# Optimization experiments

Measured on AMD Instinct MI355X. Metric: run time of the kernel, lower is better.

The kernel has to match this reference:

```python
import jax, jax.numpy as jnp
import numpy as np
from jax import lax

B, S, W = 64, 64, 12          # batch, sentences, words-per-sentence (max_seq)
V, SYM, HID = 32000, 128, 256  # vocab, symbol_size, hidden_size
E, R = 64, 32                  # entity_size, role_size
EPS = 1e-5


def _mlp(x, W1, b1, W2, b2):
    # equation 'b...e,er->b...r' is a matmul on the last axis; tanh hidden, linear out
    return jnp.tanh(x @ W1 + b1) @ W2 + b2


def _ln(x, g, b):
    mu = jnp.mean(x, axis=-1, keepdims=True)
    var = jnp.mean(jnp.square(x - mu), axis=-1, keepdims=True)
    return (x - mu) * lax.rsqrt(var + EPS) * g + b


def setup_inputs() -> dict:
    key = jax.random.key(0)
    ks = jax.random.split(key, 24)
    s_in = 1.0 / np.sqrt(SYM)
    s_h = 1.0 / np.sqrt(HID)
    inp = {
        "story": jax.random.randint(ks[0], (B, S, W), 0, V),
        "query": jax.random.randint(ks[1], (B, W), 0, V),
        "word_embed": jax.random.uniform(ks[2], (V, SYM), jnp.float32, -0.1, 0.1),
        "pos_embed": jnp.ones((W, SYM), jnp.float32) / W,
        # UpdateModule MLPs: 2 entity heads (out=E), 3 role heads (out=R), stacked
        "ue_W1": jax.random.normal(ks[3], (2, SYM, HID)) * s_in,
        "ue_b1": jnp.zeros((2, HID), jnp.float32),
        "ue_W2": jax.random.normal(ks[4], (2, HID, E)) * s_h,
        "ue_b2": jnp.zeros((2, E), jnp.float32),
        "ur_W1": jax.random.normal(ks[5], (3, SYM, HID)) * s_in,
        "ur_b1": jnp.zeros((3, HID), jnp.float32),
        "ur_W2": jax.random.normal(ks[6], (3, HID, R)) * s_h,
        "ur_b2": jnp.zeros((3, R), jnp.float32),
        # InferenceModule MLPs
        "ie_W1": jax.random.normal(ks[7], (2, SYM, HID)) * s_in,
        "ie_b1": jnp.zeros((2, HID), jnp.float32),
        "ie_W2": jax.random.normal(ks[8], (2, HID, E)) * s_h,
        "ie_b2": jnp.zeros((2, E), jnp.float32),
        "ir_W1": jax.random.normal(ks[9], (3, SYM, HID)) * s_in,
        "ir_b1": jnp.zeros((3, HID), jnp.float32),
        "ir_W2": jax.random.normal(ks[10], (3, HID, R)) * s_h,
        "ir_b2": jnp.zeros((3, R), jnp.float32),
        "ln_g": jnp.ones((3, E), jnp.float32),
        "ln_b": jnp.zeros((3, E), jnp.float32),
        "Z": jax.random.normal(ks[11], (E, V)) * (1.0 / np.sqrt(E)),
    }
    return inp


def reference(story, query, word_embed, pos_embed,
              ue_W1, ue_b1, ue_W2, ue_b2, ur_W1, ur_b1, ur_W2, ur_b2,
              ie_W1, ie_b1, ie_W2, ie_b2, ir_W1, ir_b1, ir_W2, ir_b2,
              ln_g, ln_b, Z):
    # ---- InputModule ----
    sent = jnp.einsum('bswe,we->bse', word_embed[story], pos_embed)   # [B,S,SYM]
    qsum = jnp.einsum('bwe,we->be', word_embed[query], pos_embed)     # [B,SYM]

    # ---- UpdateModule: precompute per-step entity/role vectors ----
    e1 = _mlp(sent, ue_W1[0], ue_b1[0], ue_W2[0], ue_b2[0])  # [B,S,E]
    e2 = _mlp(sent, ue_W1[1], ue_b1[1], ue_W2[1], ue_b2[1])
    r1 = _mlp(sent, ur_W1[0], ur_b1[0], ur_W2[0], ur_b2[0])  # [B,S,R]
    r2 = _mlp(sent, ur_W1[1], ur_b1[1], ur_W2[1], ur_b2[1])
    r3 = _mlp(sent, ur_W1[2], ur_b1[2], ur_W2[2], ur_b2[2])
    paW = jnp.einsum('bsr,bsf->bsrf', r1, e2)
    paB = jnp.einsum('bsr,bsf->bsrf', r3, e1)

    xs = tuple(jnp.moveaxis(t, 1, 0) for t in (e1, r1, paW, e2, r2, paB, r3))

    def step(TPR, x):
        e1i, r1i, paWi, e2i, r2i, paBi, r3i = x
        t1 = jnp.einsum('be,berf->brf', e1i, TPR)
        w_hat = jnp.einsum('br,brf->bf', r1i, t1)
        m_hat = jnp.einsum('br,brf->bf', r2i, t1)
        b_hat = jnp.einsum('be,br,berf->bf', e2i, r3i, TPR)
        write_op = paWi - r1i[:, :, None] * w_hat[:, None, :]
        move_op = r2i[:, :, None] * (w_hat - m_hat)[:, None, :]
        back_op = paBi - r3i[:, :, None] * b_hat[:, None, :]
        delta = (jnp.einsum('be,brf->berf', e1i, write_op + move_op)
                 + jnp.einsum('be,brf->berf', e2i, back_op))
        return TPR + delta, None

    TPR0 = jnp.zeros((sent.shape[0], E, R, E), sent.dtype)
    TPR, _ = lax.scan(step, TPR0, xs)

    # ---- InferenceModule ----
    qe1 = _mlp(qsum, ie_W1[0], ie_b1[0], ie_W2[0], ie_b2[0])
    qr1 = _mlp(qsum, ir_W1[0], ir_b1[0], ir_W2[0], ir_b2[0])
    qr2 = _mlp(qsum, ir_W1[1], ir_b1[1], ir_W2[1], ir_b2[1])
    qr3 = _mlp(qsum, ir_W1[2], ir_b1[2], ir_W2[2], ir_b2[2])
    i1 = _ln(jnp.einsum('be,br,berf->bf', qe1, qr1, TPR), ln_g[0], ln_b[0])
    i2 = _ln(jnp.einsum('be,br,berf->bf', i1, qr2, TPR), ln_g[1], ln_b[1])
    i3 = _ln(jnp.einsum('be,br,berf->bf', i2, qr3, TPR), ln_g[2], ln_b[2])
    return (i1 + i2 + i3) @ Z
```

## Files before the change

kernel.cpp:

```cpp
#include <hip/hip_runtime.h>
#include <math.h>

#define B_   64
#define S_   64
#define W_   12
#define V_   32000
#define SYM_ 128
#define HID_ 256
#define E_   64
#define R_   32

__global__ __launch_bounds__(128) void k_embed(
    const int* __restrict__ story, const int* __restrict__ query,
    const float* __restrict__ we, const float* __restrict__ pe,
    float* __restrict__ X) {
  int row = blockIdx.x;
  int e = threadIdx.x;
  const int* idx = (row < 4096) ? story + row * W_ : query + (row - 4096) * W_;
  float acc = 0.f;
#pragma unroll
  for (int w = 0; w < W_; ++w)
    acc = fmaf(we[(long)idx[w] * SYM_ + e], pe[w * SYM_ + e], acc);
  X[row * SYM_ + e] = acc;
}

__global__ __launch_bounds__(256) void k_mlp(
    const float* __restrict__ X,
    const float* __restrict__ ueW1, const float* __restrict__ ueb1,
    const float* __restrict__ ueW2, const float* __restrict__ ueb2,
    const float* __restrict__ urW1, const float* __restrict__ urb1,
    const float* __restrict__ urW2, const float* __restrict__ urb2,
    const float* __restrict__ ieW1, const float* __restrict__ ieb1,
    const float* __restrict__ ieW2, const float* __restrict__ ieb2,
    const float* __restrict__ irW1, const float* __restrict__ irb1,
    const float* __restrict__ irW2, const float* __restrict__ irb2,
    float* __restrict__ oE0, float* __restrict__ oE1,
    float* __restrict__ oR0, float* __restrict__ oR1, float* __restrict__ oR2) {
  __shared__ float SM[9344];
  float* W1L = SM + 1152;

  int h = blockIdx.x % 5;
  int tile = blockIdx.x / 5;
  int rowbase = tile * 32;
  bool isQ = (rowbase >= 4096);
  bool isE = (h < 2);
  const float* W1 = isE ? (isQ ? ieW1 : ueW1) + h * (SYM_ * HID_)
                        : (isQ ? irW1 : urW1) + (h - 2) * (SYM_ * HID_);
  const float* b1 = isE ? (isQ ? ieb1 : ueb1) + h * HID_
                        : (isQ ? irb1 : urb1) + (h - 2) * HID_;
  const float* W2 = isE ? (isQ ? ieW2 : ueW2) + h * (HID_ * E_)
                        : (isQ ? irW2 : urW2) + (h - 2) * (HID_ * R_);
  const float* b2 = isE ? (isQ ? ieb2 : ueb2) + h * E_
                        : (isQ ? irb2 : urb2) + (h - 2) * R_;
  float* out = (h == 0) ? oE0 : (h == 1) ? oE1 : (h == 2) ? oR0 : (h == 3) ? oR1 : oR2;

  int tid = threadIdx.x;
  int tr = tid >> 5;
  int tc = tid & 31;

  float a[4][8];
#pragma unroll
  for (int i = 0; i < 4; ++i)
#pragma unroll
    for (int j = 0; j < 8; ++j) a[i][j] = 0.f;

  for (int kc = 0; kc < 4; ++kc) {
    __syncthreads();
    {
      int i = tid;
      int row = i >> 3, k4 = (i & 7) * 4;
      float4 v = *(const float4*)(X + (long)(rowbase + row) * SYM_ + kc * 32 + k4);
      SM[(k4 + 0) * 36 + row] = v.x;
      SM[(k4 + 1) * 36 + row] = v.y;
      SM[(k4 + 2) * 36 + row] = v.z;
      SM[(k4 + 3) * 36 + row] = v.w;
    }
    {
      const float* src = W1 + kc * 32 * HID_;
#pragma unroll
      for (int i = 0; i < 8; ++i)
        *(float4*)&W1L[(tid + 256 * i) * 4] = *(const float4*)(src + (tid + 256 * i) * 4);
    }
    __syncthreads();
#pragma unroll 4
    for (int k = 0; k < 32; ++k) {
      float4 xa = *(const float4*)&SM[k * 36 + 4 * tr];
      float4 w0 = *(const float4*)&W1L[k * 256 + 8 * tc];
      float4 w1 = *(const float4*)&W1L[k * 256 + 8 * tc + 4];
      float xs[4] = {xa.x, xa.y, xa.z, xa.w};
      float ws[8] = {w0.x, w0.y, w0.z, w0.w, w1.x, w1.y, w1.z, w1.w};
#pragma unroll
      for (int i = 0; i < 4; ++i)
#pragma unroll
        for (int j = 0; j < 8; ++j) a[i][j] = fmaf(xs[i], ws[j], a[i][j]);
    }
  }
  __syncthreads();
  {
    float4 bA = *(const float4*)(b1 + 8 * tc);
    float4 bB = *(const float4*)(b1 + 8 * tc + 4);
    float b1s[8] = {bA.x, bA.y, bA.z, bA.w, bB.x, bB.y, bB.z, bB.w};
#pragma unroll
    for (int j = 0; j < 8; ++j) {
      float4 hv = make_float4(tanhf(a[0][j] + b1s[j]), tanhf(a[1][j] + b1s[j]),
                              tanhf(a[2][j] + b1s[j]), tanhf(a[3][j] + b1s[j]));
      *(float4*)&SM[(8 * tc + j) * 36 + 4 * tr] = hv;
    }
  }
  __syncthreads();
  int r0 = rowbase + 4 * tr;
  if (isE) {
    float acc0[4] = {}, acc1[4] = {};
#pragma unroll 4
    for (int c = 0; c < 256; ++c) {
      float4 h4 = *(const float4*)&SM[c * 36 + 4 * tr];
      float2 w2 = *(const float2*)(W2 + (long)c * E_ + 2 * tc);
      float hs[4] = {h4.x, h4.y, h4.z, h4.w};
#pragma unroll
      for (int i = 0; i < 4; ++i) {
        acc0[i] = fmaf(hs[i], w2.x, acc0[i]);
        acc1[i] = fmaf(hs[i], w2.y, acc1[i]);
      }
    }
    float2 b2v = *(const float2*)(b2 + 2 * tc);
#pragma unroll
    for (int i = 0; i < 4; ++i)
      *(float2*)(out + (long)(r0 + i) * E_ + 2 * tc) =
          make_float2(acc0[i] + b2v.x, acc1[i] + b2v.y);
  } else {
    float acc0[4] = {};
#pragma unroll 4
    for (int c = 0; c < 256; ++c) {
      float4 h4 = *(const float4*)&SM[c * 36 + 4 * tr];
      float w = W2[(long)c * R_ + tc];
      float hs[4] = {h4.x, h4.y, h4.z, h4.w};
#pragma unroll
      for (int i = 0; i < 4; ++i) acc0[i] = fmaf(hs[i], w, acc0[i]);
    }
    float b2v = b2[tc];
#pragma unroll
    for (int i = 0; i < 4; ++i)
      out[(long)(r0 + i) * R_ + tc] = acc0[i] + b2v;
  }
}

__global__ __launch_bounds__(256) void k_gram(
    const float* __restrict__ e1, const float* __restrict__ e2,
    const float* __restrict__ r1, const float* __restrict__ r2,
    const float* __restrict__ r3, float* __restrict__ Wt) {
  int b = blockIdx.x / 9, m = blockIdx.x % 9;
  const float* sE = ((m < 6) ? e1 : e2) + (long)b * S_ * E_;
  const float* jE = ((m == 2 || m == 5 || m == 8) ? e2 : e1) + (long)b * S_ * E_;
  int sk = m / 3, jk = m % 3;
  const float* sR = ((sk == 0) ? r1 : (sk == 1) ? r2 : r3) + (long)b * S_ * R_;
  const float* jR = ((jk == 0) ? r1 : (jk == 1) ? r2 : r3) + (long)b * S_ * R_;

  __shared__ float Es[64][68], Ej[64][68], Rs[64][36], Rj[64][36];
  int tid = threadIdx.x;
  for (int i = tid; i < 1024; i += 256) {
    int row = i >> 4, c = i & 15;
    *(float4*)&Es[row][4 * c] = *(const float4*)(sE + row * 64 + 4 * c);
    *(float4*)&Ej[row][4 * c] = *(const float4*)(jE + row * 64 + 4 * c);
  }
  for (int i = tid; i < 512; i += 256) {
    int row = i >> 3, c = i & 7;
    *(float4*)&Rs[row][4 * c] = *(const float4*)(sR + row * 32 + 4 * c);
    *(float4*)&Rj[row][4 * c] = *(const float4*)(jR + row * 32 + 4 * c);
  }
  __syncthreads();

  int s0 = (tid & 15) * 4, j0 = (tid >> 4) * 4;
  float ed[4][4] = {}, rd[4][4] = {};
#pragma unroll 4
  for (int k = 0; k < 16; ++k) {
    float4 es[4], ej[4];
#pragma unroll
    for (int i = 0; i < 4; ++i) {
      es[i] = *(const float4*)&Es[s0 + i][4 * k];
      ej[i] = *(const float4*)&Ej[j0 + i][4 * k];
    }
#pragma unroll
    for (int i = 0; i < 4; ++i)
#pragma unroll
      for (int j = 0; j < 4; ++j)
        ed[i][j] = fmaf(es[i].x, ej[j].x, fmaf(es[i].y, ej[j].y,
                   fmaf(es[i].z, ej[j].z, fmaf(es[i].w, ej[j].w, ed[i][j]))));
  }
#pragma unroll 4
  for (int k = 0; k < 8; ++k) {
    float4 rs[4], rj[4];
#pragma unroll
    for (int i = 0; i < 4; ++i) {
      rs[i] = *(const float4*)&Rs[s0 + i][4 * k];
      rj[i] = *(const float4*)&Rj[j0 + i][4 * k];
    }
#pragma unroll
    for (int i = 0; i < 4; ++i)
#pragma unroll
      for (int j = 0; j < 4; ++j)
        rd[i][j] = fmaf(rs[i].x, rj[j].x, fmaf(rs[i].y, rj[j].y,
                   fmaf(rs[i].z, rj[j].z, fmaf(rs[i].w, rj[j].w, rd[i][j]))));
  }
  float* wout = Wt + (long)(b * 9 + m) * 4096;
#pragma unroll
  for (int jj = 0; jj < 4; ++jj) {
    float4 o4 = make_float4(ed[0][jj] * rd[0][jj], ed[1][jj] * rd[1][jj],
                            ed[2][jj] * rd[2][jj], ed[3][jj] * rd[3][jj]);
    *(float4*)(wout + (j0 + jj) * 64 + s0) = o4;
  }
}

__global__ __launch_bounds__(256) void k_scan(
    const float* __restrict__ e1g, const float* __restrict__ e2g,
    const float* __restrict__ Wt, float4* __restrict__ acd) {
  __shared__ float WtL[9 * 512];
  int b = blockIdx.x & 63;
  int g = blockIdx.x >> 6;
  int tid = threadIdx.x;
  int wv = tid >> 6;
  int lane = tid & 63;
  int f0 = g * 8 + wv * 2;
  int f1 = f0 + 1;
  const float* Wb = Wt + (long)b * 9 * 4096;
  long eoff = ((long)b * 64 + lane) * 64;
  float e1x = e1g[eoff + f0], e1y = e1g[eoff + f1];
  float e2x = e2g[eoff + f0], e2y = e2g[eoff + f1];

  float pW0 = 0.f, pM0 = 0.f, pB0 = 0.f;
  float pW1 = 0.f, pM1 = 0.f, pB1 = 0.f;
  float ca0 = e2x, cc0 = 0.f, cd0 = e1x;
  float ca1 = e2y, cc1 = 0.f, cd1 = e1y;
  float ka0 = 0.f, kc0 = 0.f, kd0 = 0.f;
  float ka1 = 0.f, kc1 = 0.f, kd1 = 0.f;

  for (int jc = 0; jc < 8; ++jc) {
    __syncthreads();
    for (int i = tid; i < 1152; i += 256) {
      int m = i >> 7;
      int off = (i & 127) * 4;
      *(float4*)&WtL[m * 512 + off] = *(const float4*)(Wb + m * 4096 + jc * 512 + off);
    }
    __syncthreads();
#pragma unroll
    for (int jj = 0; jj < 8; ++jj) {
      int j = jc * 8 + jj;
      float wa = WtL[0 * 512 + jj * 64 + lane];
      float wc = WtL[1 * 512 + jj * 64 + lane];
      float wd = WtL[2 * 512 + jj * 64 + lane];
      float ma = WtL[3 * 512 + jj * 64 + lane];
      float mc = WtL[4 * 512 + jj * 64 + lane];
      float md = WtL[5 * 512 + jj * 64 + lane];
      float ba = WtL[6 * 512 + jj * 64 + lane];
      float bc = WtL[7 * 512 + jj * 64 + lane];
      float bd = WtL[8 * 512 + jj * 64 + lane];
      float aj0 = __int_as_float(__builtin_amdgcn_readlane(__float_as_int(ca0), j));
      float cj0 = __int_as_float(__builtin_amdgcn_readlane(__float_as_int(cc0), j));
      float dj0 = __int_as_float(__builtin_amdgcn_readlane(__float_as_int(cd0), j));
      float aj1 = __int_as_float(__builtin_amdgcn_readlane(__float_as_int(ca1), j));
      float cj1 = __int_as_float(__builtin_amdgcn_readlane(__float_as_int(cc1), j));
      float dj1 = __int_as_float(__builtin_amdgcn_readlane(__float_as_int(cd1), j));
      bool own = (lane == j);
      ka0 = own ? ca0 : ka0; kc0 = own ? cc0 : kc0; kd0 = own ? cd0 : kd0;
      ka1 = own ? ca1 : ka1; kc1 = own ? cc1 : kc1; kd1 = own ? cd1 : kd1;
      pW0 = fmaf(wa, aj0, pW0); pW0 = fmaf(wc, cj0, pW0); pW0 = fmaf(wd, dj0, pW0);
      pM0 = fmaf(ma, aj0, pM0); pM0 = fmaf(mc, cj0, pM0); pM0 = fmaf(md, dj0, pM0);
      pB0 = fmaf(ba, aj0, pB0); pB0 = fmaf(bc, cj0, pB0); pB0 = fmaf(bd, dj0, pB0);
      pW1 = fmaf(wa, aj1, pW1); pW1 = fmaf(wc, cj1, pW1); pW1 = fmaf(wd, dj1, pW1);
      pM1 = fmaf(ma, aj1, pM1); pM1 = fmaf(mc, cj1, pM1); pM1 = fmaf(md, dj1, pM1);
      pB1 = fmaf(ba, aj1, pB1); pB1 = fmaf(bc, cj1, pB1); pB1 = fmaf(bd, dj1, pB1);
      ca0 = e2x - pW0; cc0 = pW0 - pM0; cd0 = e1x - pB0;
      ca1 = e2y - pW1; cc1 = pW1 - pM1; cd1 = e1y - pB1;
    }
  }
  acd[eoff + f0] = make_float4(ka0, kc0, kd0, 0.f);
  acd[eoff + f1] = make_float4(ka1, kc1, kd1, 0.f);
}

__global__ __launch_bounds__(1024) void k_infer(
    const float4* __restrict__ acd,
    const float* __restrict__ e1, const float* __restrict__ e2,
    const float* __restrict__ r1, const float* __restrict__ r2,
    const float* __restrict__ r3,
    const float* __restrict__ qe1, const float* __restrict__ qr1,
    const float* __restrict__ qr2, const float* __restrict__ qr3,
    const float* __restrict__ lng, const float* __restrict__ lnb,
    float* __restrict__ isum) {
  int b = blockIdx.x, tid = threadIdx.x;
  __shared__ float hista[64 * 65], histc[64 * 65], histd[64 * 65];
  __shared__ float vlds[9 * 64];
  __shared__ float ivec[64];
  __shared__ float u1s[64], u2s[64];
  __shared__ float dsc[64];

  {
    const float4* ab = acd + (long)b * 4096;
    for (int idx = tid; idx < 4096; idx += 1024) {
      float4 hv = ab[idx];
      int j = idx >> 6, f = idx & 63;
      hista[j * 65 + f] = hv.x;
      histc[j * 65 + f] = hv.y;
      histd[j * 65 + f] = hv.z;
    }
  }
  if (tid < 576) {
    int pk = tid >> 6, j = tid & 63;
    int p = pk / 3, k = pk % 3;
    const float* rv = ((k == 0) ? r1 : (k == 1) ? r2 : r3) + ((long)b * 64 + j) * 32;
    const float* q = ((p == 0) ? qr1 : (p == 1) ? qr2 : qr3) + b * 32;
    float acc = 0.f;
#pragma unroll
    for (int t = 0; t < 8; ++t) {
      float4 rv4 = *(const float4*)(rv + 4 * t);
      float4 q4 = *(const float4*)(q + 4 * t);
      acc = fmaf(rv4.x, q4.x, fmaf(rv4.y, q4.y,
            fmaf(rv4.z, q4.z, fmaf(rv4.w, q4.w, acc))));
    }
    vlds[pk * 64 + j] = acc;
  }
  if (tid < 64) ivec[tid] = qe1[b * 64 + tid];
  __syncthreads();

  int f = tid >> 4, jsl = tid & 15;
  int dotd = tid >> 3, dt = tid & 7;
  int which = dotd >> 6, dj = dotd & 63;
  const float* erow = (which ? e2 : e1) + ((long)b * 64 + dj) * 64 + dt * 8;
  float isacc = 0.f;
  for (int p = 0; p < 3; ++p) {
    {
      float acc = 0.f;
#pragma unroll
      for (int t = 0; t < 8; ++t)
        acc = fmaf(erow[t], ivec[dt * 8 + t], acc);
      acc += __shfl_xor(acc, 1, 64);
      acc += __shfl_xor(acc, 2, 64);
      acc += __shfl_xor(acc, 4, 64);
      if (dt == 0) { if (which) u2s[dj] = acc; else u1s[dj] = acc; }
    }
    __syncthreads();
    float part = 0.f;
#pragma unroll
    for (int i = 0; i < 4; ++i) {
      int j = jsl * 4 + i;
      float ca = u1s[j] * vlds[(p * 3 + 0) * 64 + j];
      float cc = u1s[j] * vlds[(p * 3 + 1) * 64 + j];
      float cd = u2s[j] * vlds[(p * 3 + 2) * 64 + j];
      part = fmaf(ca, hista[j * 65 + f],
             fmaf(cc, histc[j * 65 + f],
             fmaf(cd, histd[j * 65 + f], part)));
    }
    part += __shfl_xor(part, 1, 64);
    part += __shfl_xor(part, 2, 64);
    part += __shfl_xor(part, 4, 64);
    part += __shfl_xor(part, 8, 64);
    if (jsl == 0) dsc[f] = part;
    __syncthreads();
    if (tid < 64) {
      float v = dsc[tid];
      float mu = v;
#pragma unroll
      for (int mm = 1; mm <= 32; mm <<= 1) mu += __shfl_xor(mu, mm, 64);
      mu *= (1.f / 64.f);
      float d = v - mu;
      float vr = d * d;
#pragma unroll
      for (int mm = 1; mm <= 32; mm <<= 1) vr += __shfl_xor(vr, mm, 64);
      vr *= (1.f / 64.f);
      float iv = d * (1.f / sqrtf(vr + 1e-5f)) * lng[p * 64 + tid] + lnb[p * 64 + tid];
      ivec[tid] = iv;
      isacc += iv;
    }
    __syncthreads();
  }
  if (tid < 64) isum[b * 64 + tid] = isacc;
}

__global__ __launch_bounds__(256) void k_final(
    const float* __restrict__ isum, const float* __restrict__ Zm,
    float* __restrict__ out) {
  __shared__ float isT[64 * 68];
  int tid = threadIdx.x;
  for (int i = tid; i < 4096; i += 256) {
    int bb = i >> 6, e = i & 63;
    isT[e * 68 + bb] = isum[i];
  }
  __syncthreads();
  int tr = tid >> 4, tc = tid & 15;
  int v0 = blockIdx.x * 64 + tc * 4;
  float acc[4][4] = {};
#pragma unroll 2
  for (int e = 0; e < 64; ++e) {
    float4 a4 = *(const float4*)&isT[e * 68 + 4 * tr];
    float4 z4 = *(const float4*)(Zm + (long)e * V_ + v0);
    float as[4] = {a4.x, a4.y, a4.z, a4.w};
    float zs[4] = {z4.x, z4.y, z4.z, z4.w};
#pragma unroll
    for (int i = 0; i < 4; ++i)
#pragma unroll
      for (int j = 0; j < 4; ++j) acc[i][j] = fmaf(as[i], zs[j], acc[i][j]);
  }
#pragma unroll
  for (int i = 0; i < 4; ++i) {
    float4 o4 = make_float4(acc[i][0], acc[i][1], acc[i][2], acc[i][3]);
    *(float4*)(out + (long)(4 * tr + i) * V_ + v0) = o4;
  }
}

extern "C" void kernel_launch(void* const* d_in, const int* in_sizes, int n_in,
                              void* d_out, int out_size, void* d_ws, size_t ws_size,
                              hipStream_t stream) {
  const int* story = (const int*)d_in[0];
  const int* query = (const int*)d_in[1];
  const float* we = (const float*)d_in[2];
  const float* pe = (const float*)d_in[3];
  const float* ueW1 = (const float*)d_in[4];
  const float* ueb1 = (const float*)d_in[5];
  const float* ueW2 = (const float*)d_in[6];
  const float* ueb2 = (const float*)d_in[7];
  const float* urW1 = (const float*)d_in[8];
  const float* urb1 = (const float*)d_in[9];
  const float* urW2 = (const float*)d_in[10];
  const float* urb2 = (const float*)d_in[11];
  const float* ieW1 = (const float*)d_in[12];
  const float* ieb1 = (const float*)d_in[13];
  const float* ieW2 = (const float*)d_in[14];
  const float* ieb2 = (const float*)d_in[15];
  const float* irW1 = (const float*)d_in[16];
  const float* irb1 = (const float*)d_in[17];
  const float* irW2 = (const float*)d_in[18];
  const float* irb2 = (const float*)d_in[19];
  const float* lng = (const float*)d_in[20];
  const float* lnb = (const float*)d_in[21];
  const float* Zm = (const float*)d_in[22];

  float* ws = (float*)d_ws;
  float* X = ws;
  float* e1 = X + 532480;
  float* e2 = e1 + 266240;
  float* r1 = e2 + 266240;
  float* r2 = r1 + 133120;
  float* r3 = r2 + 133120;
  float* isum = r3 + 133120;
  float* Wt = isum + 4096;
  float4* acd = (float4*)(Wt + 2359296);
  float* qe1 = e1 + 4096 * 64;
  float* qr1 = r1 + 4096 * 32;
  float* qr2 = r2 + 4096 * 32;
  float* qr3 = r3 + 4096 * 32;
  float* outF = (float*)d_out;

  k_embed<<<4160, 128, 0, stream>>>(story, query, we, pe, X);
  k_mlp<<<130 * 5, 256, 0, stream>>>(X, ueW1, ueb1, ueW2, ueb2,
                                     urW1, urb1, urW2, urb2,
                                     ieW1, ieb1, ieW2, ieb2,
                                     irW1, irb1, irW2, irb2,
                                     e1, e2, r1, r2, r3);
  k_gram<<<64 * 9, 256, 0, stream>>>(e1, e2, r1, r2, r3, Wt);
  k_scan<<<512, 256, 0, stream>>>(e1, e2, Wt, acd);
  k_infer<<<B_, 1024, 0, stream>>>(acd, e1, e2, r1, r2, r3, qe1, qr1, qr2, qr3,
                                   lng, lnb, isum);
  k_final<<<V_ / 64, 256, 0, stream>>>(isum, Zm, outF);
}
```

Baseline: 223.8 us.

## Remap MLP kernel threads so each wave owns rows and lanes own columns

Reorganises the fused MLP kernel so each 64-lane wave handles 8 rows and each lane handles 4 hidden columns. Activation and hidden values are now read from shared memory as wave-uniform broadcasts, and the second layer reads W2 coalesced across lanes. The shared-memory padding changes to 40 and 260 floats per row to suit the new access pattern. For the 32-wide role heads, half of each wave computes duplicate results that are never stored, so some arithmetic is wasted.

```diff
diff --git a/kernel.cpp b/kernel.cpp
--- a/kernel.cpp
+++ b/kernel.cpp
@@ -36,8 +36,8 @@
     const float* __restrict__ irW2, const float* __restrict__ irb2,
     float* __restrict__ oE0, float* __restrict__ oE1,
     float* __restrict__ oR0, float* __restrict__ oR1, float* __restrict__ oR2) {
-  __shared__ float SM[9344];
-  float* W1L = SM + 1152;
+  __shared__ float SM[9472];
+  float* W1L = SM + 1280;
 
   int h = blockIdx.x % 5;
   int tile = blockIdx.x / 5;
@@ -55,92 +55,101 @@
   float* out = (h == 0) ? oE0 : (h == 1) ? oE1 : (h == 2) ? oR0 : (h == 3) ? oR1 : oR2;
 
   int tid = threadIdx.x;
-  int tr = tid >> 5;
-  int tc = tid & 31;
-
-  float a[4][8];
-#pragma unroll
-  for (int i = 0; i < 4; ++i)
-#pragma unroll
-    for (int j = 0; j < 8; ++j) a[i][j] = 0.f;
+  int wv = tid >> 6;
+  int l = tid & 63;
+
+  float a[8][4];
+#pragma unroll
+  for (int i = 0; i < 8; ++i)
+#pragma unroll
+    for (int q = 0; q < 4; ++q) a[i][q] = 0.f;
 
   for (int kc = 0; kc < 4; ++kc) {
     __syncthreads();
     {
-      int i = tid;
-      int row = i >> 3, k4 = (i & 7) * 4;
+      int row = tid >> 3, k4 = (tid & 7) * 4;
       float4 v = *(const float4*)(X + (long)(rowbase + row) * SYM_ + kc * 32 + k4);
-      SM[(k4 + 0) * 36 + row] = v.x;
-      SM[(k4 + 1) * 36 + row] = v.y;
-      SM[(k4 + 2) * 36 + row] = v.z;
-      SM[(k4 + 3) * 36 + row] = v.w;
+      SM[(k4 + 0) * 40 + row] = v.x;
+      SM[(k4 + 1) * 40 + row] = v.y;
+      SM[(k4 + 2) * 40 + row] = v.z;
+      SM[(k4 + 3) * 40 + row] = v.w;
     }
     {
       const float* src = W1 + kc * 32 * HID_;
 #pragma unroll
-      for (int i = 0; i < 8; ++i)
-        *(float4*)&W1L[(tid + 256 * i) * 4] = *(const float4*)(src + (tid + 256 * i) * 4);
+      for (int t = 0; t < 8; ++t)
+        *(float4*)&W1L[(tid + 256 * t) * 4] = *(const float4*)(src + (tid + 256 * t) * 4);
     }
     __syncthreads();
 #pragma unroll 4
     for (int k = 0; k < 32; ++k) {
-      float4 xa = *(const float4*)&SM[k * 36 + 4 * tr];
-      float4 w0 = *(const float4*)&W1L[k * 256 + 8 * tc];
-      float4 w1 = *(const float4*)&W1L[k * 256 + 8 * tc + 4];
-      float xs[4] = {xa.x, xa.y, xa.z, xa.w};
-      float ws[8] = {w0.x, w0.y, w0.z, w0.w, w1.x, w1.y, w1.z, w1.w};
-#pragma unroll
-      for (int i = 0; i < 4; ++i)
-#pragma unroll
-        for (int j = 0; j < 8; ++j) a[i][j] = fmaf(xs[i], ws[j], a[i][j]);
+      float4 wvv = *(const float4*)&W1L[k * 256 + 4 * l];
+      float4 x0 = *(const float4*)&SM[k * 40 + 8 * wv];
+      float4 x1 = *(const float4*)&SM[k * 40 + 8 * wv + 4];
+      float xs[8] = {x0.x, x0.y, x0.z, x0.w, x1.x, x1.y, x1.z, x1.w};
+#pragma unroll
+      for (int i = 0; i < 8; ++i) {
+        a[i][0] = fmaf(xs[i], wvv.x, a[i][0]);
+        a[i][1] = fmaf(xs[i], wvv.y, a[i][1]);
+        a[i][2] = fmaf(xs[i], wvv.z, a[i][2]);
+        a[i][3] = fmaf(xs[i], wvv.w, a[i][3]);
+      }
     }
   }
   __syncthreads();
   {
-    float4 bA = *(const float4*)(b1 + 8 * tc);
-    float4 bB = *(const float4*)(b1 + 8 * tc + 4);
-    float b1s[8] = {bA.x, bA.y, bA.z, bA.w, bB.x, bB.y, bB.z, bB.w};
-#pragma unroll
-    for (int j = 0; j < 8; ++j) {
-      float4 hv = make_float4(tanhf(a[0][j] + b1s[j]), tanhf(a[1][j] + b1s[j]),
-                              tanhf(a[2][j] + b1s[j]), tanhf(a[3][j] + b1s[j]));
-      *(float4*)&SM[(8 * tc + j) * 36 + 4 * tr] = hv;
+    float4 b1v = *(const float4*)(b1 + 4 * l);
+#pragma unroll
+    for (int i = 0; i < 8; ++i) {
+      float4 hv = make_float4(tanhf(a[i][0] + b1v.x), tanhf(a[i][1] + b1v.y),
+                              tanhf(a[i][2] + b1v.z), tanhf(a[i][3] + b1v.w));
+      *(float4*)&SM[(8 * wv + i) * 260 + 4 * l] = hv;
     }
   }
   __syncthreads();
-  int r0 = rowbase + 4 * tr;
   if (isE) {
-    float acc0[4] = {}, acc1[4] = {};
-#pragma unroll 4
-    for (int c = 0; c < 256; ++c) {
-      float4 h4 = *(const float4*)&SM[c * 36 + 4 * tr];
-      float2 w2 = *(const float2*)(W2 + (long)c * E_ + 2 * tc);
-      float hs[4] = {h4.x, h4.y, h4.z, h4.w};
-#pragma unroll
-      for (int i = 0; i < 4; ++i) {
-        acc0[i] = fmaf(hs[i], w2.x, acc0[i]);
-        acc1[i] = fmaf(hs[i], w2.y, acc1[i]);
+    float acc[8];
+#pragma unroll
+    for (int i = 0; i < 8; ++i) acc[i] = 0.f;
+#pragma unroll 2
+    for (int c4 = 0; c4 < 64; ++c4) {
+      float w0 = W2[(long)(4 * c4 + 0) * E_ + l];
+      float w1 = W2[(long)(4 * c4 + 1) * E_ + l];
+      float w2 = W2[(long)(4 * c4 + 2) * E_ + l];
+      float w3 = W2[(long)(4 * c4 + 3) * E_ + l];
+#pragma unroll
+      for (int i = 0; i < 8; ++i) {
+        float4 hh = *(const float4*)&SM[(8 * wv + i) * 260 + 4 * c4];
+        acc[i] = fmaf(hh.x, w0, fmaf(hh.y, w1, fmaf(hh.z, w2, fmaf(hh.w, w3, acc[i]))));
       }
     }
-    float2 b2v = *(const float2*)(b2 + 2 * tc);
-#pragma unroll
-    for (int i = 0; i < 4; ++i)
-      *(float2*)(out + (long)(r0 + i) * E_ + 2 * tc) =
-          make_float2(acc0[i] + b2v.x, acc1[i] + b2v.y);
+    float bb = b2[l];
+#pragma unroll
+    for (int i = 0; i < 8; ++i)
+      out[(long)(rowbase + 8 * wv + i) * E_ + l] = acc[i] + bb;
   } else {
-    float acc0[4] = {};
-#pragma unroll 4
-    for (int c = 0; c < 256; ++c) {
-      float4 h4 = *(const float4*)&SM[c * 36 + 4 * tr];
-      float w = W2[(long)c * R_ + tc];
-      float hs[4] = {h4.x, h4.y, h4.z, h4.w};
-#pragma unroll
-      for (int i = 0; i < 4; ++i) acc0[i] = fmaf(hs[i], w, acc0[i]);
-    }
-    float b2v = b2[tc];
-#pragma unroll
-    for (int i = 0; i < 4; ++i)
-      out[(long)(r0 + i) * R_ + tc] = acc0[i] + b2v;
+    int lc = l & 31;
+    float acc[8];
+#pragma unroll
+    for (int i = 0; i < 8; ++i) acc[i] = 0.f;
+#pragma unroll 2
+    for (int c4 = 0; c4 < 64; ++c4) {
+      float w0 = W2[(long)(4 * c4 + 0) * R_ + lc];
+      float w1 = W2[(long)(4 * c4 + 1) * R_ + lc];
+      float w2 = W2[(long)(4 * c4 + 2) * R_ + lc];
+      float w3 = W2[(long)(4 * c4 + 3) * R_ + lc];
+#pragma unroll
+      for (int i = 0; i < 8; ++i) {
+        float4 hh = *(const float4*)&SM[(8 * wv + i) * 260 + 4 * c4];
+        acc[i] = fmaf(hh.x, w0, fmaf(hh.y, w1, fmaf(hh.z, w2, fmaf(hh.w, w3, acc[i]))));
+      }
+    }
+    if (l < 32) {
+      float bb = b2[lc];
+#pragma unroll
+      for (int i = 0; i < 8; ++i)
+        out[(long)(rowbase + 8 * wv + i) * R_ + lc] = acc[i] + bb;
+    }
   }
 }
 
```

New measurement: 221.9 us. No clear change (-0.9%).
